# Kernel optimization log

Hardware: AMD Instinct MI355X
Metric: run time of the kernel (lower is better)

The kernel has to match this reference:

```python
import jax, jax.numpy as jnp
import numpy as np

B, SW, SE, D, H, FF = 8, 512, 128, 1024, 16, 4096
HD = D // H
EPS = 1e-12
SCALE = 1.0 / np.sqrt(HD).astype(np.float32)


def _split_heads(x):
    # [B, S, D] -> [B, H, S, HD]
    b, s, _ = x.shape
    return x.reshape(b, s, H, HD).transpose(0, 2, 1, 3)


def _layer_norm(x, g, b):
    m = jnp.mean(x, axis=-1, keepdims=True)
    v = jnp.mean(jnp.square(x - m), axis=-1, keepdims=True)
    return g * (x - m) / jnp.sqrt(v + EPS) + b


def setup_inputs() -> dict:
    key = jax.random.key(0)
    ks = iter(jax.random.split(key, 40))
    std = 0.02

    def w(i, o):
        return jax.random.normal(next(ks), (i, o), jnp.float32) * std

    inp = {
        "word_hidden_states": jax.random.normal(next(ks), (B, SW, D), jnp.float32),
        "entity_hidden_states": jax.random.normal(next(ks), (B, SE, D), jnp.float32),
        "word_attention_mask": jnp.zeros((B, SW), jnp.float32),
        "entity_attention_mask": jnp.zeros((B, SE), jnp.float32),
        # entity-aware self attention projections
        "Wq": w(D, D), "bq": jnp.zeros((D,), jnp.float32),
        "Ww2e": w(D, D), "bw2e": jnp.zeros((D,), jnp.float32),
        "We2w": w(D, D), "be2w": jnp.zeros((D,), jnp.float32),
        "We2e": w(D, D), "be2e": jnp.zeros((D,), jnp.float32),
        "Wk": w(D, D), "bk": jnp.zeros((D,), jnp.float32),
        "Wv": w(D, D), "bv": jnp.zeros((D,), jnp.float32),
        # BertSelfOutput
        "Wo": w(D, D), "bo": jnp.zeros((D,), jnp.float32),
        "ln1_g": jnp.ones((D,), jnp.float32), "ln1_b": jnp.zeros((D,), jnp.float32),
        # BertIntermediate / BertOutput
        "Wi": w(D, FF), "bi": jnp.zeros((FF,), jnp.float32),
        "Wout": w(FF, D), "bout": jnp.zeros((D,), jnp.float32),
        "ln2_g": jnp.ones((D,), jnp.float32), "ln2_b": jnp.zeros((D,), jnp.float32),
    }
    return inp


def _layer(wh, eh, wmask, emask, Wq, bq, Ww2e, bw2e, We2w, be2w, We2e, be2e,
           Wk, bk, Wv, bv, Wo, bo, ln1_g, ln1_b, Wi, bi, Wout, bout, ln2_g, ln2_b):
    sw = wh.shape[1]
    hidden = jnp.concatenate([wh, eh], axis=1)              # [B, S, D]
    mask = jnp.concatenate([wmask, emask], axis=-1)[:, None, None, :]  # additive

    q_w2w = _split_heads(wh @ Wq + bq)
    q_w2e = _split_heads(wh @ Ww2e + bw2e)
    q_e2w = _split_heads(eh @ We2w + be2w)
    q_e2e = _split_heads(eh @ We2e + be2e)
    k = _split_heads(hidden @ Wk + bk)                      # [B, H, S, HD]
    kw, ke = k[:, :, :sw, :], k[:, :, sw:, :]

    s_w2w = jnp.einsum("bhqd,bhkd->bhqk", q_w2w, kw)
    s_w2e = jnp.einsum("bhqd,bhkd->bhqk", q_w2e, ke)
    s_e2w = jnp.einsum("bhqd,bhkd->bhqk", q_e2w, kw)
    s_e2e = jnp.einsum("bhqd,bhkd->bhqk", q_e2e, ke)
    word_scores = jnp.concatenate([s_w2w, s_w2e], axis=3)
    ent_scores = jnp.concatenate([s_e2w, s_e2e], axis=3)
    scores = jnp.concatenate([word_scores, ent_scores], axis=2) * SCALE + mask
    probs = jax.nn.softmax(scores, axis=-1)

    v = _split_heads(hidden @ Wv + bv)
    ctx = jnp.einsum("bhqk,bhkd->bhqd", probs, v)
    ctx = ctx.transpose(0, 2, 1, 3).reshape(wh.shape[0], -1, D)  # [B, S, D]

    # BertSelfOutput: dense + residual + LN
    attn_out = _layer_norm(ctx @ Wo + bo + hidden, ln1_g, ln1_b)
    # BertIntermediate + BertOutput
    inter = jax.nn.gelu(attn_out @ Wi + bi, approximate=False)
    out = _layer_norm(inter @ Wout + bout + attn_out, ln2_g, ln2_b)
    return out[:, :sw, :], out[:, sw:, :]


def reference(word_hidden_states, entity_hidden_states, word_attention_mask,
              entity_attention_mask, Wq, bq, Ww2e, bw2e, We2w, be2w, We2e, be2e,
              Wk, bk, Wv, bv, Wo, bo, ln1_g, ln1_b, Wi, bi, Wout, bout,
              ln2_g, ln2_b):
    return _layer(word_hidden_states, entity_hidden_states, word_attention_mask,
                  entity_attention_mask, Wq, bq, Ww2e, bw2e, We2w, be2w, We2e,
                  be2e, Wk, bk, Wv, bv, Wo, bo, ln1_g, ln1_b, Wi, bi, Wout,
                  bout, ln2_g, ln2_b)
```

## Files before the change

kernel.cpp:

```cpp
#include <hip/hip_runtime.h>
#include <hip/hip_bf16.h>
#include <stdint.h>
#include <math.h>

#define DEV __device__ __forceinline__

using bf16 = __hip_bfloat16;
typedef __attribute__((ext_vector_type(8))) short bf16x8;
typedef __attribute__((ext_vector_type(4))) float f32x4;

static constexpr int NB  = 8;
static constexpr int NSW = 512;
static constexpr int NSE = 128;
static constexpr int ND  = 1024;
static constexpr int NH  = 16;
static constexpr int NFF = 4096;
static constexpr int NS  = NSW + NSE;
static constexpr int NHD = 64;

DEV f32x4 mfma16(bf16x8 a, bf16x8 b, f32x4 c){
  return __builtin_amdgcn_mfma_f32_16x16x32_bf16(a, b, c, 0, 0, 0);
}

DEV void gload16(const bf16* g, bf16* l){
  __builtin_amdgcn_global_load_lds((const __attribute__((address_space(1))) void*)g,
                                   (__attribute__((address_space(3))) void*)l,
                                   16, 0, 0);
}

DEV bf16 tobf(float f){ return __float2bfloat16(f); }

union PK4 { bf16 h[4]; short4 s; };

__global__ __launch_bounds__(256) void cast_word_k(const float* __restrict__ wh,
                                                   bf16* __restrict__ whb,
                                                   bf16* __restrict__ hid){
  long i = ((long)blockIdx.x*256 + threadIdx.x)*4;
  float4 v = *reinterpret_cast<const float4*>(wh + i);
  PK4 p; p.h[0]=tobf(v.x); p.h[1]=tobf(v.y); p.h[2]=tobf(v.z); p.h[3]=tobf(v.w);
  *reinterpret_cast<short4*>(whb + i) = p.s;
  long row = i >> 10; int c = (int)(i & 1023);
  int b = (int)(row >> 9), s = (int)(row & 511);
  *reinterpret_cast<short4*>(hid + ((long)(b*NS + s) << 10) + c) = p.s;
}

__global__ __launch_bounds__(256) void cast_ent_k(const float* __restrict__ eh,
                                                  bf16* __restrict__ ehb,
                                                  bf16* __restrict__ hid){
  long i = ((long)blockIdx.x*256 + threadIdx.x)*4;
  float4 v = *reinterpret_cast<const float4*>(eh + i);
  PK4 p; p.h[0]=tobf(v.x); p.h[1]=tobf(v.y); p.h[2]=tobf(v.z); p.h[3]=tobf(v.w);
  *reinterpret_cast<short4*>(ehb + i) = p.s;
  long row = i >> 10; int c = (int)(i & 1023);
  int b = (int)(row >> 7), s = (int)(row & 127);
  *reinterpret_cast<short4*>(hid + ((long)(b*NS + NSW + s) << 10) + c) = p.s;
}

struct TP7 { const float* src[7]; bf16* dst[7]; };

__global__ void transpose7_k(TP7 tp){
  __shared__ float tile[32][33];
  const float* in = tp.src[blockIdx.z];
  bf16* out = tp.dst[blockIdx.z];
  const int c0 = blockIdx.x*32, r0 = blockIdx.y*32;
  const int tx = threadIdx.x, ty = threadIdx.y;
  #pragma unroll
  for (int i=0;i<4;i++)
    tile[ty + i*8][tx] = in[(long)(r0 + ty + i*8)*1024 + c0 + tx];
  __syncthreads();
  #pragma unroll
  for (int i=0;i<4;i++){
    int rr = ty + i*8;
    out[(long)(c0 + rr)*1024 + r0 + tx] = tobf(tile[tx][rr]);
  }
}

__global__ void transpose_cast_k(const float* __restrict__ in, bf16* __restrict__ out,
                                 int R, int C){
  __shared__ float tile[32][33];
  const int c0 = blockIdx.x*32, r0 = blockIdx.y*32;
  const int tx = threadIdx.x, ty = threadIdx.y;
  #pragma unroll
  for (int i=0;i<4;i++)
    tile[ty + i*8][tx] = in[(long)(r0 + ty + i*8)*C + c0 + tx];
  __syncthreads();
  #pragma unroll
  for (int i=0;i<4;i++){
    int rr = ty + i*8;
    out[(long)(c0 + rr)*R + r0 + tx] = tobf(tile[tx][rr]);
  }
}

__global__ void bias_concat_k(const float* __restrict__ bq, const float* __restrict__ bw2e,
                              const float* __restrict__ be2w, const float* __restrict__ be2e,
                              const float* __restrict__ bk, const float* __restrict__ bv,
                              float* __restrict__ bQw, float* __restrict__ bQe,
                              float* __restrict__ bKV){
  int i = blockIdx.x*256 + threadIdx.x;
  bQw[i] = bq[i];   bQw[1024+i] = bw2e[i];
  bQe[i] = be2w[i]; bQe[1024+i] = be2e[i];
  bKV[i] = bk[i];   bKV[1024+i] = bv[i];
}

template<int EPI>
__global__ __launch_bounds__(256) void gemm_bt_k(const bf16* __restrict__ A,
                                                 const bf16* __restrict__ Bt,
                                                 const float* __restrict__ bias,
                                                 void* __restrict__ Cout,
                                                 void* __restrict__ Cout2,
                                                 int M, int N, int K){
  __shared__ __align__(16) bf16 As[128*64];
  __shared__ __align__(16) bf16 Bs[128*64];
  const int tid = threadIdx.x;

  const int nwg = gridDim.x*gridDim.y;
  const int orig = blockIdx.y*gridDim.x + blockIdx.x;
  const int qq = nwg >> 3, rr8 = nwg & 7;
  const int xcd = orig & 7, idx = orig >> 3;
  const int wg = (xcd < rr8 ? xcd*(qq+1) : rr8*(qq+1) + (xcd-rr8)*qq) + idx;
  const int m0 = (wg / gridDim.x)*128, n0 = (wg % gridDim.x)*128;

  const int wid = tid>>6, lane = tid&63;
  const int wr = wid>>1, wc = wid&1;
  const int lr = lane&15, lg = lane>>4;

  const f32x4 zero = {0.f,0.f,0.f,0.f};
  f32x4 acc[4][4];
  #pragma unroll
  for (int m=0;m<4;m++)
    #pragma unroll
    for (int n=0;n<4;n++) acc[m][n] = zero;

  for (int kt=0; kt<K; kt+=64){
    #pragma unroll
    for (int i=0;i<4;i++){
      int idx2 = i*256 + tid;
      int row = idx2>>3, kc = idx2&7;
      gload16(A + (long)(m0+row)*K + kt + kc*8, As + idx2*8);
    }
    #pragma unroll
    for (int i=0;i<4;i++){
      int idx2 = i*256 + tid;
      int row = idx2>>3, kc = idx2&7;
      gload16(Bt + (long)(n0+row)*K + kt + kc*8, Bs + idx2*8);
    }
    __syncthreads();
    #pragma unroll
    for (int ks=0; ks<2; ks++){
      bf16x8 af[4], bg[4];
      #pragma unroll
      for (int m=0;m<4;m++)
        af[m] = *reinterpret_cast<const bf16x8*>(As + (wr*64 + m*16 + lr)*64 + ks*32 + lg*8);
      #pragma unroll
      for (int n=0;n<4;n++)
        bg[n] = *reinterpret_cast<const bf16x8*>(Bs + (wc*64 + n*16 + lr)*64 + ks*32 + lg*8);
      __builtin_amdgcn_s_setprio(1);
      #pragma unroll
      for (int m=0;m<4;m++)
        #pragma unroll
        for (int n=0;n<4;n++)
          acc[m][n] = mfma16(af[m], bg[n], acc[m][n]);
      __builtin_amdgcn_s_setprio(0);
    }
    __syncthreads();
  }

  #pragma unroll
  for (int m=0;m<4;m++){
    const int rbase = m0 + wr*64 + m*16 + lg*4;
    #pragma unroll
    for (int n=0;n<4;n++){
      const int col = n0 + wc*64 + n*16 + lr;
      const float bsv = bias[col];
      #pragma unroll
      for (int r=0;r<4;r++){
        const int rw = rbase + r;
        float v = acc[m][n][r] + bsv;
        if constexpr (EPI == 0){
          ((bf16*)Cout)[(long)rw*N + col] = tobf(v);
        } else if constexpr (EPI == 2){
          ((float*)Cout)[(long)rw*N + col] = v;
        } else if constexpr (EPI == 3){
          float ge = 0.5f*v*(1.0f + erff(v*0.70710678118654752f));
          ((bf16*)Cout)[(long)rw*N + col] = tobf(ge);
        } else {
          if (col < 1024){
            ((bf16*)Cout)[(long)rw*2048 + col] = tobf(v);
          } else {
            int bb = rw / NS, ss = rw % NS, hh = (col-1024) >> 6, dd = (col-1024) & 63;
            ((bf16*)Cout2)[((long)((bb*NH + hh)*NHD + dd))*NS + ss] = tobf(v);
          }
        }
      }
    }
  }
}

__global__ __launch_bounds__(256) void attn_k(
    const bf16* __restrict__ Qw,
    const bf16* __restrict__ Qe,
    const bf16* __restrict__ KV,
    const bf16* __restrict__ Vt,
    const float* __restrict__ wm, const float* __restrict__ em,
    bf16* __restrict__ ctx){
  __shared__ __align__(16) bf16 Plds[4][2][16*40];
  const int tid = threadIdx.x, wid = tid>>6, lane = tid&63;
  const int lr = lane&15, lg = lane>>4;
  const int w   = blockIdx.x*4 + wid;
  const int b   = w / (NH*20);
  const int rem = w % (NH*20);
  const int h   = rem / 20;
  const int q0  = (rem % 20)*32;

  const bf16* Qbase; long qrow0;
  if (q0 < NSW){ Qbase = Qw; qrow0 = (long)b*NSW + q0; }
  else         { Qbase = Qe; qrow0 = (long)b*NSE + (q0 - NSW); }

  bf16x8 qA[2][2], qB[2][2];
  #pragma unroll
  for (int m=0;m<2;m++)
    #pragma unroll
    for (int dc=0; dc<2; dc++){
      long o = (qrow0 + m*16 + lr)*2048 + h*NHD + dc*32 + lg*8;
      qA[m][dc] = *reinterpret_cast<const bf16x8*>(Qbase + o);
      qB[m][dc] = *reinterpret_cast<const bf16x8*>(Qbase + o + 1024);
    }

  const f32x4 zero = {0.f,0.f,0.f,0.f};
  f32x4 cacc[2][4];
  float mrow[2][4], lsum[2][4];
  #pragma unroll
  for (int m=0;m<2;m++){
    #pragma unroll
    for (int dt=0;dt<4;dt++) cacc[m][dt] = zero;
    #pragma unroll
    for (int r=0;r<4;r++){ mrow[m][r] = -1e30f; lsum[m][r] = 0.f; }
  }

  const bf16* Kbase = KV + (long)b*NS*2048 + h*NHD;
  const bf16* Vbase = Vt + (long)((b*NH + h)*NHD)*NS;

  for (int kt=0; kt<20; kt++){
    const int k0 = kt*32;
    const bool word = (k0 < NSW);

    bf16x8 kf[2][2], vf[4];
    #pragma unroll
    for (int sub=0;sub<2;sub++)
      #pragma unroll
      for (int dc=0;dc<2;dc++)
        kf[sub][dc] = *reinterpret_cast<const bf16x8*>(
            Kbase + (long)(k0 + sub*16 + lr)*2048 + dc*32 + lg*8);
    #pragma unroll
    for (int dt=0;dt<4;dt++)
      vf[dt] = *reinterpret_cast<const bf16x8*>(
          Vbase + (long)(dt*16 + lr)*NS + k0 + lg*8);

    float msk0, msk1;
    { int k = k0 + lr;
      msk0 = word ? wm[b*NSW + k]      : em[b*NSE + (k - NSW)];
      msk1 = word ? wm[b*NSW + k + 16] : em[b*NSE + (k + 16 - NSW)];
    }

    f32x4 sc[2][2];
    #pragma unroll
    for (int m=0;m<2;m++){ sc[m][0]=zero; sc[m][1]=zero; }
    __builtin_amdgcn_s_setprio(1);
    #pragma unroll
    for (int m=0;m<2;m++)
      #pragma unroll
      for (int sub=0;sub<2;sub++)
        #pragma unroll
        for (int dc=0;dc<2;dc++){
          const bf16x8 q = word ? qA[m][dc] : qB[m][dc];
          sc[m][sub] = mfma16(q, kf[sub][dc], sc[m][sub]);
        }
    __builtin_amdgcn_s_setprio(0);

    #pragma unroll
    for (int m=0;m<2;m++){
      bf16* pw = &Plds[wid][m][0];
      #pragma unroll
      for (int r=0;r<4;r++){
        float s0 = sc[m][0][r]*0.125f + msk0;
        float s1 = sc[m][1][r]*0.125f + msk1;
        float t = fmaxf(s0, s1);
        #pragma unroll
        for (int o=8;o;o>>=1) t = fmaxf(t, __shfl_xor(t, o, 16));
        float mn = fmaxf(mrow[m][r], t);
        float al = __expf(mrow[m][r] - mn);
        mrow[m][r] = mn;
        float p0 = __expf(s0 - mn), p1 = __expf(s1 - mn);
        float ps = p0 + p1;
        #pragma unroll
        for (int o=8;o;o>>=1) ps += __shfl_xor(ps, o, 16);
        lsum[m][r] = lsum[m][r]*al + ps;
        pw[(lg*4+r)*40 + lr]      = tobf(p0);
        pw[(lg*4+r)*40 + 16 + lr] = tobf(p1);
        #pragma unroll
        for (int dt=0;dt<4;dt++) cacc[m][dt][r] *= al;
      }
    }

    __builtin_amdgcn_s_setprio(1);
    #pragma unroll
    for (int m=0;m<2;m++){
      bf16x8 pa = *reinterpret_cast<const bf16x8*>(&Plds[wid][m][0] + lr*40 + lg*8);
      #pragma unroll
      for (int dt=0;dt<4;dt++)
        cacc[m][dt] = mfma16(pa, vf[dt], cacc[m][dt]);
    }
    __builtin_amdgcn_s_setprio(0);
  }

  #pragma unroll
  for (int m=0;m<2;m++)
    #pragma unroll
    for (int r=0;r<4;r++){
      float inv = 1.f/lsum[m][r];
      #pragma unroll
      for (int dt=0;dt<4;dt++) cacc[m][dt][r] *= inv;
    }
  long crow = (long)b*NS + q0;
  #pragma unroll
  for (int m=0;m<2;m++)
    #pragma unroll
    for (int dt=0;dt<4;dt++)
      #pragma unroll
      for (int r=0;r<4;r++)
        ctx[(crow + m*16 + lg*4 + r)*ND + h*NHD + dt*16 + lr] = tobf(cacc[m][dt][r]);
}

DEV void block_red2(float& s1, float& s2){
  __shared__ float red[8];
  #pragma unroll
  for (int o=32;o;o>>=1){ s1 += __shfl_down(s1,o); s2 += __shfl_down(s2,o); }
  int wid = threadIdx.x>>6, lane = threadIdx.x&63;
  if (lane==0){ red[wid]=s1; red[4+wid]=s2; }
  __syncthreads();
  s1 = red[0]+red[1]+red[2]+red[3];
  s2 = red[4]+red[5]+red[6]+red[7];
}

__global__ __launch_bounds__(256) void ln1_k(const float* __restrict__ ctxO,
    const float* __restrict__ wh, const float* __restrict__ eh,
    const float* __restrict__ g, const float* __restrict__ be,
    float* __restrict__ outF, bf16* __restrict__ outB){
  const int row = blockIdx.x;
  const int b = row / NS, s = row % NS;
  const float* resid = (s < NSW) ? wh + ((long)(b*NSW + s))*ND
                                 : eh + ((long)(b*NSE + (s-NSW)))*ND;
  const int t = threadIdx.x;
  float4 xv = reinterpret_cast<const float4*>(ctxO + (long)row*ND)[t];
  float4 rv = reinterpret_cast<const float4*>(resid)[t];
  float4 x = make_float4(xv.x+rv.x, xv.y+rv.y, xv.z+rv.z, xv.w+rv.w);
  float s1 = x.x+x.y+x.z+x.w;
  float s2 = x.x*x.x + x.y*x.y + x.z*x.z + x.w*x.w;
  block_red2(s1, s2);
  float mean = s1 * (1.f/ND);
  float var  = s2 * (1.f/ND) - mean*mean;
  float rstd = rsqrtf(var + 1e-12f);
  float4 gv = reinterpret_cast<const float4*>(g)[t];
  float4 bv = reinterpret_cast<const float4*>(be)[t];
  float4 y = make_float4(gv.x*(x.x-mean)*rstd + bv.x,
                         gv.y*(x.y-mean)*rstd + bv.y,
                         gv.z*(x.z-mean)*rstd + bv.z,
                         gv.w*(x.w-mean)*rstd + bv.w);
  reinterpret_cast<float4*>(outF + (long)row*ND)[t] = y;
  PK4 p; p.h[0]=tobf(y.x); p.h[1]=tobf(y.y); p.h[2]=tobf(y.z); p.h[3]=tobf(y.w);
  reinterpret_cast<short4*>(outB + (long)row*ND)[t] = p.s;
}

__global__ __launch_bounds__(256) void ln2_k(const float* __restrict__ ffo,
    const float* __restrict__ attnF, const float* __restrict__ g,
    const float* __restrict__ be, float* __restrict__ out){
  const int row = blockIdx.x;
  const int b = row / NS, s = row % NS;
  const int t = threadIdx.x;
  float4 xv = reinterpret_cast<const float4*>(ffo + (long)row*ND)[t];
  float4 rv = reinterpret_cast<const float4*>(attnF + (long)row*ND)[t];
  float4 x = make_float4(xv.x+rv.x, xv.y+rv.y, xv.z+rv.z, xv.w+rv.w);
  float s1 = x.x+x.y+x.z+x.w;
  float s2 = x.x*x.x + x.y*x.y + x.z*x.z + x.w*x.w;
  block_red2(s1, s2);
  float mean = s1 * (1.f/ND);
  float var  = s2 * (1.f/ND) - mean*mean;
  float rstd = rsqrtf(var + 1e-12f);
  float4 gv = reinterpret_cast<const float4*>(g)[t];
  float4 bv = reinterpret_cast<const float4*>(be)[t];
  float4 y = make_float4(gv.x*(x.x-mean)*rstd + bv.x,
                         gv.y*(x.y-mean)*rstd + bv.y,
                         gv.z*(x.z-mean)*rstd + bv.z,
                         gv.w*(x.w-mean)*rstd + bv.w);
  float* op = (s < NSW) ? out + ((long)(b*NSW+s))*ND
                        : out + (long)NB*NSW*ND + ((long)(b*NSE + (s-NSW)))*ND;
  reinterpret_cast<float4*>(op)[t] = y;
}

extern "C" void kernel_launch(void* const* d_in, const int* in_sizes, int n_in,
                              void* d_out, int out_size, void* d_ws, size_t ws_size,
                              hipStream_t stream){
  (void)in_sizes; (void)n_in; (void)out_size; (void)ws_size;
  const float* wh   = (const float*)d_in[0];
  const float* eh   = (const float*)d_in[1];
  const float* wm   = (const float*)d_in[2];
  const float* em   = (const float*)d_in[3];
  const float* Wq   = (const float*)d_in[4];   const float* bq   = (const float*)d_in[5];
  const float* Ww2e = (const float*)d_in[6];   const float* bw2e = (const float*)d_in[7];
  const float* We2w = (const float*)d_in[8];   const float* be2w = (const float*)d_in[9];
  const float* We2e = (const float*)d_in[10];  const float* be2e = (const float*)d_in[11];
  const float* Wk   = (const float*)d_in[12];  const float* bk   = (const float*)d_in[13];
  const float* Wv   = (const float*)d_in[14];  const float* bv   = (const float*)d_in[15];
  const float* Wo   = (const float*)d_in[16];  const float* bo   = (const float*)d_in[17];
  const float* g1   = (const float*)d_in[18];  const float* b1   = (const float*)d_in[19];
  const float* Wi   = (const float*)d_in[20];  const float* bi   = (const float*)d_in[21];
  const float* Wout = (const float*)d_in[22];  const float* bout = (const float*)d_in[23];
  const float* g2   = (const float*)d_in[24];  const float* b2   = (const float*)d_in[25];
  float* out = (float*)d_out;

  char* ws = (char*)d_ws;
  size_t off = 0;
  auto alloc = [&](size_t bytes)->char*{
    char* p = ws + off; off += (bytes + 255) & ~(size_t)255; return p;
  };

  bf16* hid   = (bf16*)alloc((size_t)NB*NS*ND*2);
  bf16* whb   = (bf16*)alloc((size_t)NB*NSW*ND*2);
  bf16* ehb   = (bf16*)alloc((size_t)NB*NSE*ND*2);
  bf16* WqwT  = (bf16*)alloc((size_t)2048*ND*2);
  bf16* WqeT  = (bf16*)alloc((size_t)2048*ND*2);
  bf16* WkvT  = (bf16*)alloc((size_t)2048*ND*2);
  bf16* WoT   = (bf16*)alloc((size_t)ND*ND*2);
  bf16* WiT   = (bf16*)alloc((size_t)NFF*ND*2);
  bf16* WoutT = (bf16*)alloc((size_t)ND*NFF*2);
  float* bQw  = (float*)alloc(2048*4);
  float* bQe  = (float*)alloc(2048*4);
  float* bKV  = (float*)alloc(2048*4);

  char* u1 = alloc((size_t)52428800);
  bf16* Qwb = (bf16*)u1;
  bf16* Qeb = Qwb + (size_t)NB*NSW*2048;
  bf16* KVb = Qeb + (size_t)NB*NSE*2048;
  bf16* Vt  = KVb + (size_t)NB*NS*2048;
  bf16* inter = (bf16*)u1;
  bf16* attnB = (bf16*)(u1 + (size_t)41943040);

  bf16*  ctx   = (bf16*)alloc((size_t)NB*NS*ND*2);
  float* ctxO  = (float*)alloc((size_t)NB*NS*ND*4);
  float* ffo   = ctxO;
  float* attnF = (float*)alloc((size_t)NB*NS*ND*4);

  dim3 tb(32,8);
  cast_word_k<<<4096, 256, 0, stream>>>(wh, whb, hid);
  cast_ent_k <<<1024, 256, 0, stream>>>(eh, ehb, hid);

  TP7 tp;
  tp.src[0]=Wq;   tp.dst[0]=WqwT;
  tp.src[1]=Ww2e; tp.dst[1]=WqwT + (size_t)1024*1024;
  tp.src[2]=We2w; tp.dst[2]=WqeT;
  tp.src[3]=We2e; tp.dst[3]=WqeT + (size_t)1024*1024;
  tp.src[4]=Wk;   tp.dst[4]=WkvT;
  tp.src[5]=Wv;   tp.dst[5]=WkvT + (size_t)1024*1024;
  tp.src[6]=Wo;   tp.dst[6]=WoT;
  transpose7_k<<<dim3(32,32,7), tb, 0, stream>>>(tp);
  transpose_cast_k<<<dim3(128,32), tb, 0, stream>>>(Wi,   WiT,   ND, NFF);
  transpose_cast_k<<<dim3(32,128), tb, 0, stream>>>(Wout, WoutT, NFF, ND);
  bias_concat_k<<<4, 256, 0, stream>>>(bq, bw2e, be2w, be2e, bk, bv, bQw, bQe, bKV);

  gemm_bt_k<0><<<dim3(16,32), 256, 0, stream>>>(whb, WqwT, bQw, Qwb, nullptr, NB*NSW, 2048, ND);
  gemm_bt_k<0><<<dim3(16, 8), 256, 0, stream>>>(ehb, WqeT, bQe, Qeb, nullptr, NB*NSE, 2048, ND);
  gemm_bt_k<4><<<dim3(16,40), 256, 0, stream>>>(hid, WkvT, bKV, KVb, Vt,      NB*NS,  2048, ND);

  attn_k<<<640, 256, 0, stream>>>(Qwb, Qeb, KVb, Vt, wm, em, ctx);

  gemm_bt_k<2><<<dim3(8,40),  256, 0, stream>>>(ctx,   WoT,   bo,   ctxO,  nullptr, NB*NS, ND,  ND);
  ln1_k<<<5120, 256, 0, stream>>>(ctxO, wh, eh, g1, b1, attnF, attnB);
  gemm_bt_k<3><<<dim3(32,40), 256, 0, stream>>>(attnB, WiT,   bi,   inter, nullptr, NB*NS, NFF, ND);
  gemm_bt_k<2><<<dim3(8,40),  256, 0, stream>>>(inter, WoutT, bout, ffo,   nullptr, NB*NS, ND,  NFF);
  ln2_k<<<5120, 256, 0, stream>>>(ffo, attnF, g2, b2, out);
}
```

Before: 605.9 us.

## Split-K for N=1024 GEMMs and split-KV across waves in attention

The two N=1024 output GEMMs now run with a 2-way split-K grid, writing fp32 partial sums to two buffers that are added inside the LayerNorm kernels. The second partial buffer reuses the hidden-state bf16 workspace, which is dead by then. Attention now gives each workgroup one query tile and splits the 20 key tiles across its 4 waves, merging softmax max, sum and accumulators through LDS. The aim is to raise parallelism and occupancy on under-filled grids, at the cost of extra partial-sum traffic and LDS reduction with barriers.

```diff
diff --git a/kernel.cpp b/kernel.cpp
--- a/kernel.cpp
+++ b/kernel.cpp
@@ -120,6 +120,9 @@
   const int wg = (xcd < rr8 ? xcd*(qq+1) : rr8*(qq+1) + (xcd-rr8)*qq) + idx;
   const int m0 = (wg / gridDim.x)*128, n0 = (wg % gridDim.x)*128;
 
+  const int Kc  = K / gridDim.z;
+  const int kt0 = blockIdx.z * Kc;
+
   const int wid = tid>>6, lane = tid&63;
   const int wr = wid>>1, wc = wid&1;
   const int lr = lane&15, lg = lane>>4;
@@ -131,7 +134,7 @@
     #pragma unroll
     for (int n=0;n<4;n++) acc[m][n] = zero;
 
-  for (int kt=0; kt<K; kt+=64){
+  for (int kt=kt0; kt<kt0+Kc; kt+=64){
     #pragma unroll
     for (int i=0;i<4;i++){
       int idx2 = i*256 + tid;
@@ -171,25 +174,26 @@
     #pragma unroll
     for (int n=0;n<4;n++){
       const int col = n0 + wc*64 + n*16 + lr;
-      const float bsv = bias[col];
+      const float bsv = (EPI == 5 && blockIdx.z != 0) ? 0.f : bias[col];
       #pragma unroll
       for (int r=0;r<4;r++){
         const int rw = rbase + r;
         float v = acc[m][n][r] + bsv;
         if constexpr (EPI == 0){
           ((bf16*)Cout)[(long)rw*N + col] = tobf(v);
-        } else if constexpr (EPI == 2){
-          ((float*)Cout)[(long)rw*N + col] = v;
         } else if constexpr (EPI == 3){
           float ge = 0.5f*v*(1.0f + erff(v*0.70710678118654752f));
           ((bf16*)Cout)[(long)rw*N + col] = tobf(ge);
-        } else {
+        } else if constexpr (EPI == 4){
           if (col < 1024){
             ((bf16*)Cout)[(long)rw*2048 + col] = tobf(v);
           } else {
             int bb = rw / NS, ss = rw % NS, hh = (col-1024) >> 6, dd = (col-1024) & 63;
             ((bf16*)Cout2)[((long)((bb*NH + hh)*NHD + dd))*NS + ss] = tobf(v);
           }
+        } else {
+          float* dst = blockIdx.z == 0 ? (float*)Cout : (float*)Cout2;
+          dst[(long)rw*N + col] = v;
         }
       }
     }
@@ -204,9 +208,12 @@
     const float* __restrict__ wm, const float* __restrict__ em,
     bf16* __restrict__ ctx){
   __shared__ __align__(16) bf16 Plds[4][2][16*40];
+  __shared__ float mred[4][2][16];
+  __shared__ float lred[4][2][16];
+  __shared__ __align__(16) float accred[4][16][64];
   const int tid = threadIdx.x, wid = tid>>6, lane = tid&63;
   const int lr = lane&15, lg = lane>>4;
-  const int w   = blockIdx.x*4 + wid;
+  const int w   = blockIdx.x;
   const int b   = w / (NH*20);
   const int rem = w % (NH*20);
   const int h   = rem / 20;
@@ -240,7 +247,7 @@
   const bf16* Kbase = KV + (long)b*NS*2048 + h*NHD;
   const bf16* Vbase = Vt + (long)((b*NH + h)*NHD)*NS;
 
-  for (int kt=0; kt<20; kt++){
+  for (int kt=wid*5; kt<wid*5+5; kt++){
     const int k0 = kt*32;
     const bool word = (k0 < NSW);
 
@@ -316,19 +323,49 @@
   #pragma unroll
   for (int m=0;m<2;m++)
     #pragma unroll
+    for (int r=0;r<4;r++)
+      if (lr == 0){
+        mred[wid][m][lg*4+r] = mrow[m][r];
+        lred[wid][m][lg*4+r] = lsum[m][r];
+      }
+  __syncthreads();
+
+  float Lg[2][4], scl[2][4];
+  #pragma unroll
+  for (int m=0;m<2;m++)
+    #pragma unroll
     for (int r=0;r<4;r++){
-      float inv = 1.f/lsum[m][r];
-      #pragma unroll
-      for (int dt=0;dt<4;dt++) cacc[m][dt][r] *= inv;
-    }
-  long crow = (long)b*NS + q0;
-  #pragma unroll
-  for (int m=0;m<2;m++)
+      const int row = lg*4 + r;
+      float M0 = fmaxf(fmaxf(mred[0][m][row], mred[1][m][row]),
+                       fmaxf(mred[2][m][row], mred[3][m][row]));
+      float lt = 0.f;
+      #pragma unroll
+      for (int ww=0; ww<4; ww++)
+        lt += lred[ww][m][row] * __expf(mred[ww][m][row] - M0);
+      Lg[m][r]  = lt;
+      scl[m][r] = __expf(mrow[m][r] - M0);
+    }
+
+  const long crow = (long)b*NS + q0;
+  #pragma unroll
+  for (int m=0;m<2;m++){
     #pragma unroll
     for (int dt=0;dt<4;dt++)
       #pragma unroll
       for (int r=0;r<4;r++)
-        ctx[(crow + m*16 + lg*4 + r)*ND + h*NHD + dt*16 + lr] = tobf(cacc[m][dt][r]);
+        accred[wid][dt*4+r][lane] = cacc[m][dt][r] * scl[m][r];
+    __syncthreads();
+    { const int dt = wid;
+      #pragma unroll
+      for (int r=0;r<4;r++){
+        float s = accred[0][dt*4+r][lane] + accred[1][dt*4+r][lane]
+                + accred[2][dt*4+r][lane] + accred[3][dt*4+r][lane];
+        s /= Lg[m][r];
+        ctx[(crow + m*16 + lg*4 + r)*ND + h*NHD + dt*16 + lr] = tobf(s);
+      }
+    }
+    __syncthreads();
+  }
 }
 
 DEV void block_red2(float& s1, float& s2){
@@ -343,6 +380,7 @@
 }
 
 __global__ __launch_bounds__(256) void ln1_k(const float* __restrict__ ctxO,
+    const float* __restrict__ ctxO1,
     const float* __restrict__ wh, const float* __restrict__ eh,
     const float* __restrict__ g, const float* __restrict__ be,
     float* __restrict__ outF, bf16* __restrict__ outB){
@@ -352,8 +390,9 @@
                                  : eh + ((long)(b*NSE + (s-NSW)))*ND;
   const int t = threadIdx.x;
   float4 xv = reinterpret_cast<const float4*>(ctxO + (long)row*ND)[t];
+  float4 x1 = reinterpret_cast<const float4*>(ctxO1 + (long)row*ND)[t];
   float4 rv = reinterpret_cast<const float4*>(resid)[t];
-  float4 x = make_float4(xv.x+rv.x, xv.y+rv.y, xv.z+rv.z, xv.w+rv.w);
+  float4 x = make_float4(xv.x+x1.x+rv.x, xv.y+x1.y+rv.y, xv.z+x1.z+rv.z, xv.w+x1.w+rv.w);
   float s1 = x.x+x.y+x.z+x.w;
   float s2 = x.x*x.x + x.y*x.y + x.z*x.z + x.w*x.w;
   block_red2(s1, s2);
@@ -372,14 +411,16 @@
 }
 
 __global__ __launch_bounds__(256) void ln2_k(const float* __restrict__ ffo,
+    const float* __restrict__ ffo1,
     const float* __restrict__ attnF, const float* __restrict__ g,
     const float* __restrict__ be, float* __restrict__ out){
   const int row = blockIdx.x;
   const int b = row / NS, s = row % NS;
   const int t = threadIdx.x;
   float4 xv = reinterpret_cast<const float4*>(ffo + (long)row*ND)[t];
+  float4 x1 = reinterpret_cast<const float4*>(ffo1 + (long)row*ND)[t];
   float4 rv = reinterpret_cast<const float4*>(attnF + (long)row*ND)[t];
-  float4 x = make_float4(xv.x+rv.x, xv.y+rv.y, xv.z+rv.z, xv.w+rv.w);
+  float4 x = make_float4(xv.x+x1.x+rv.x, xv.y+x1.y+rv.y, xv.z+x1.z+rv.z, xv.w+x1.w+rv.w);
   float s1 = x.x+x.y+x.z+x.w;
   float s2 = x.x*x.x + x.y*x.y + x.z*x.z + x.w*x.w;
   block_red2(s1, s2);
@@ -427,6 +468,7 @@
   bf16* hid   = (bf16*)alloc((size_t)NB*NS*ND*2);
   bf16* whb   = (bf16*)alloc((size_t)NB*NSW*ND*2);
   bf16* ehb   = (bf16*)alloc((size_t)NB*NSE*ND*2);
+  float* part1 = (float*)hid;
   bf16* WqwT  = (bf16*)alloc((size_t)2048*ND*2);
   bf16* WqeT  = (bf16*)alloc((size_t)2048*ND*2);
   bf16* WkvT  = (bf16*)alloc((size_t)2048*ND*2);
@@ -471,11 +513,11 @@
   gemm_bt_k<0><<<dim3(16, 8), 256, 0, stream>>>(ehb, WqeT, bQe, Qeb, nullptr, NB*NSE, 2048, ND);
   gemm_bt_k<4><<<dim3(16,40), 256, 0, stream>>>(hid, WkvT, bKV, KVb, Vt,      NB*NS,  2048, ND);
 
-  attn_k<<<640, 256, 0, stream>>>(Qwb, Qeb, KVb, Vt, wm, em, ctx);
-
-  gemm_bt_k<2><<<dim3(8,40),  256, 0, stream>>>(ctx,   WoT,   bo,   ctxO,  nullptr, NB*NS, ND,  ND);
-  ln1_k<<<5120, 256, 0, stream>>>(ctxO, wh, eh, g1, b1, attnF, attnB);
-  gemm_bt_k<3><<<dim3(32,40), 256, 0, stream>>>(attnB, WiT,   bi,   inter, nullptr, NB*NS, NFF, ND);
-  gemm_bt_k<2><<<dim3(8,40),  256, 0, stream>>>(inter, WoutT, bout, ffo,   nullptr, NB*NS, ND,  NFF);
-  ln2_k<<<5120, 256, 0, stream>>>(ffo, attnF, g2, b2, out);
-}
+  attn_k<<<2560, 256, 0, stream>>>(Qwb, Qeb, KVb, Vt, wm, em, ctx);
+
+  gemm_bt_k<5><<<dim3(8,40,2),  256, 0, stream>>>(ctx,   WoT,   bo,   ctxO, part1, NB*NS, ND,  ND);
+  ln1_k<<<5120, 256, 0, stream>>>(ctxO, part1, wh, eh, g1, b1, attnF, attnB);
+  gemm_bt_k<3><<<dim3(32,40),   256, 0, stream>>>(attnB, WiT,   bi,   inter, nullptr, NB*NS, NFF, ND);
+  gemm_bt_k<5><<<dim3(8,40,2),  256, 0, stream>>>(inter, WoutT, bout, ffo,  part1, NB*NS, ND,  NFF);
+  ln2_k<<<5120, 256, 0, stream>>>(ffo, part1, attnF, g2, b2, out);
+}
```

Measured after the change: 563.0 us. -7.1%, faster.
